# Performance work log

Hardware: AMD Instinct MI355X
Metric: run time of the kernel (lower is better)

The kernel has to match this reference:

```python
import jax, jax.numpy as jnp
import numpy as np
from jax import lax

E = 4      # n_experts
K = 2      # top_k
D = 1024   # d_model
B, S = 4, 4096


def setup_inputs() -> dict:
    key = jax.random.key(0)
    ks = jax.random.split(key, 9)
    sc = 1.0 / np.sqrt(D)
    x = jax.random.normal(ks[0], (B, S, D), dtype=jnp.float32)
    Wg = jax.random.normal(ks[1], (E, D, D), dtype=jnp.float32) * sc
    bg = jax.random.normal(ks[2], (E, D), dtype=jnp.float32) * sc
    Wv = jax.random.normal(ks[3], (E, D, D), dtype=jnp.float32) * sc
    bv = jax.random.normal(ks[4], (E, D), dtype=jnp.float32) * sc
    Wd = jax.random.normal(ks[5], (E, D, D), dtype=jnp.float32) * sc
    # decay_bias_init = 1.0 (torch init.constant_)
    bd = jnp.ones((E, D), dtype=jnp.float32)
    Wgate = jax.random.normal(ks[7], (E, D), dtype=jnp.float32) * sc
    return {"x": x, "Wg": Wg, "bg": bg, "Wv": Wv, "bv": bv,
            "Wd": Wd, "bd": bd, "Wgate": Wgate}


def reference(x, Wg, bg, Wv, bv, Wd, bd, Wgate):
    # Per-expert projections (torch Linear: y = x @ W.T + b; W is (out,in))
    g = jnp.einsum('bsd,eod->ebso', x, Wg) + bg[:, None, None, :]  # (E,B,S,D)
    v = jnp.einsum('bsd,eod->ebso', x, Wv) + bv[:, None, None, :]
    d = jnp.einsum('bsd,eod->ebso', x, Wd) + bd[:, None, None, :]
    x_scan = jax.nn.sigmoid(g) * jnp.tanh(v)
    a = 0.001 + 0.998 * jax.nn.sigmoid(d)

    # Causal linear RNN: h_t = a_t * h_{t-1} + x_t, vectorized over (E,B,D)
    xs = jnp.moveaxis(x_scan, 2, 0)  # (S,E,B,D)
    as_ = jnp.moveaxis(a, 2, 0)      # (S,E,B,D)

    def step(h, inp):
        a_t, x_t = inp
        h = a_t * h + x_t
        return h, h

    h0 = jnp.zeros((E, B, x.shape[-1]), dtype=x.dtype)
    _, outs = lax.scan(step, h0, (as_, xs))        # (S,E,B,D)
    expert_outs = jnp.transpose(outs, (2, 0, 3, 1))  # (B,S,D,E)

    # Router: top-k experts per token, softmax over selected logits
    gate_logits = jnp.einsum('bsd,ed->bse', x, Wgate)  # (B,S,E)
    top_vals, top_idx = lax.top_k(gate_logits, K)      # (B,S,K)
    weights = jax.nn.softmax(top_vals, axis=-1)        # (B,S,K)

    idx = jnp.broadcast_to(top_idx[:, :, None, :],
                           (x.shape[0], x.shape[1], x.shape[2], K))
    selected = jnp.take_along_axis(expert_outs, idx, axis=-1)  # (B,S,D,K)
    return (selected * weights[:, :, None, :]).sum(axis=-1)
```

## Files before the change

### kernel.cpp

```cpp
#include <hip/hip_runtime.h>

#define E_EXP 4
#define D_MODEL 1024
#define B_BATCH 4
#define S_SEQ 4096
#define NTOK (B_BATCH*S_SEQ)
#define CHUNK 32
#define NCHUNK (S_SEQ/CHUNK)

typedef float f4 __attribute__((ext_vector_type(4)));
typedef float f32x4 __attribute__((ext_vector_type(4)));
typedef short bf16x8 __attribute__((ext_vector_type(8)));

__device__ __forceinline__ unsigned short f2b(float f){
  union{float f;unsigned u;}v; v.f=f;
  unsigned r = v.u + 0x7fffu + ((v.u>>16)&1u);
  return (unsigned short)(r>>16);
}
__device__ __forceinline__ float b2f_lo(unsigned v){ union{unsigned u;float f;}x; x.u=v<<16; return x.f; }
__device__ __forceinline__ float b2f_hi(unsigned v){ union{unsigned u;float f;}x; x.u=v&0xffff0000u; return x.f; }

__device__ __forceinline__ void gload_lds16(const void* g, void* l){
  __builtin_amdgcn_global_load_lds(
      (const __attribute__((address_space(1))) void*)g,
      (__attribute__((address_space(3))) void*)l, 16, 0, 0);
}

__global__ __launch_bounds__(256) void cvt_bf16(const float* __restrict__ src,
                                                unsigned short* __restrict__ dst)
{
  size_t i = ((size_t)blockIdx.x*256 + threadIdx.x)*4;
  f4 v = *(const f4*)(src + i);
  ushort4 o; o.x=f2b(v[0]); o.y=f2b(v[1]); o.z=f2b(v[2]); o.w=f2b(v[3]);
  *(ushort4*)(dst + i) = o;
}

__global__ __launch_bounds__(256) void cvt_w3(const float* __restrict__ Wg,
                                              const float* __restrict__ Wv,
                                              const float* __restrict__ Wd,
                                              unsigned short* __restrict__ Wcat,
                                              int e0)
{
  const size_t DD = (size_t)D_MODEL*D_MODEL;
  size_t i4 = ((size_t)blockIdx.x*256 + threadIdx.x)*4;
  size_t le3m = i4 >> 20;
  size_t rem  = i4 & (DD-1);
  int mat = (int)(le3m % 3);
  int le  = (int)(le3m / 3);
  const float* src = (mat==0 ? Wg : (mat==1 ? Wv : Wd)) + (size_t)(e0+le)*DD + rem;
  f4 v = *(const f4*)src;
  ushort4 o; o.x=f2b(v[0]); o.y=f2b(v[1]); o.z=f2b(v[2]); o.w=f2b(v[3]);
  *(ushort4*)(Wcat + le3m*DD + rem) = o;
}

__global__ __launch_bounds__(256) void router_kernel(
    const float* __restrict__ x, const float* __restrict__ Wgate,
    float* __restrict__ wtok)
{
  int gtid = blockIdx.x*256 + threadIdx.x;
  int tok  = gtid >> 6;
  int lane = threadIdx.x & 63;
  const float* xr = x + (size_t)tok * D_MODEL;
  float acc0=0.f,acc1=0.f,acc2=0.f,acc3=0.f;
  for (int k=lane;k<D_MODEL;k+=64){
    float xv = xr[k];
    acc0 += xv*Wgate[0*D_MODEL+k];
    acc1 += xv*Wgate[1*D_MODEL+k];
    acc2 += xv*Wgate[2*D_MODEL+k];
    acc3 += xv*Wgate[3*D_MODEL+k];
  }
  #pragma unroll
  for (int off=32;off>0;off>>=1){
    acc0 += __shfl_down(acc0,off);
    acc1 += __shfl_down(acc1,off);
    acc2 += __shfl_down(acc2,off);
    acc3 += __shfl_down(acc3,off);
  }
  if (lane==0){
    float l[4]={acc0,acc1,acc2,acc3};
    int i1=0;
    #pragma unroll
    for(int e=1;e<4;e++) if (l[e]>l[i1]) i1=e;
    int i2=-1;
    #pragma unroll
    for(int e=0;e<4;e++){ if(e==i1) continue; if(i2<0||l[e]>l[i2]) i2=e; }
    float ex = __expf(l[i2]-l[i1]);
    float w1 = 1.f/(1.f+ex);
    float w2 = ex/(1.f+ex);
    float w[4]={0.f,0.f,0.f,0.f};
    w[i1]=w1; w[i2]=w2;
    float* wp = wtok + (size_t)tok*E_EXP;
    wp[0]=w[0]; wp[1]=w[1]; wp[2]=w[2]; wp[3]=w[3];
  }
}

#define BM 128
#define BN 128
#define BK 32

__global__ __launch_bounds__(256) void gemm_3n(
    const unsigned short* __restrict__ A,
    const unsigned short* __restrict__ Wcat,
    unsigned short* __restrict__ gvd)
{
  __shared__ unsigned short sA[BM*BK];
  __shared__ unsigned short sB[BN*BK];
  const size_t DD = (size_t)D_MODEL*D_MODEL;
  const size_t ND = (size_t)NTOK*D_MODEL;

  int le    = blockIdx.z;
  int mbase = blockIdx.x*BM;
  int ntile = blockIdx.y;
  int mat   = ntile>>3;
  int nbase = (ntile&7)*BN;
  int tid  = threadIdx.x;
  int wave = tid>>6, lane = tid&63;
  int wm = wave>>1, wn = wave&1;

  const unsigned short* Wmat = Wcat + ((size_t)le*3 + mat)*DD;

  int src_chunk = (lane&3) ^ ((lane>>3)&3);
  int srow = lane>>2;
  const unsigned short* gA0 = A    + (size_t)(mbase + wave*32 + srow)*D_MODEL + src_chunk*8;
  const unsigned short* gA1 = gA0  + (size_t)16*D_MODEL;
  const unsigned short* gB0 = Wmat + (size_t)(nbase + wave*32 + srow)*D_MODEL + src_chunk*8;
  const unsigned short* gB1 = gB0  + (size_t)16*D_MODEL;
  unsigned short* lA0 = &sA[(wave*32)*BK];
  unsigned short* lA1 = &sA[(wave*32+16)*BK];
  unsigned short* lB0 = &sB[(wave*32)*BK];
  unsigned short* lB1 = &sB[(wave*32+16)*BK];

  f32x4 acc[4][4];
  #pragma unroll
  for (int i=0;i<4;i++)
    #pragma unroll
    for (int j=0;j<4;j++) acc[i][j] = 0;

  int swiz   = (lane>>1)&3;
  int rd_chk = ((lane>>4) ^ swiz)*8;
  int a_base = (wm*64 + (lane&15))*BK + rd_chk;
  int b_base = (wn*64 + (lane&15))*BK + rd_chk;

  for (int k0=0; k0<D_MODEL; k0+=BK){
    gload_lds16(gA0 + k0, lA0);
    gload_lds16(gA1 + k0, lA1);
    gload_lds16(gB0 + k0, lB0);
    gload_lds16(gB1 + k0, lB1);
    __syncthreads();
    bf16x8 af[4], bfv[4];
    #pragma unroll
    for (int mi=0;mi<4;mi++) af[mi]  = *(const bf16x8*)&sA[a_base + mi*16*BK];
    #pragma unroll
    for (int ni=0;ni<4;ni++) bfv[ni] = *(const bf16x8*)&sB[b_base + ni*16*BK];
    #pragma unroll
    for (int mi=0;mi<4;mi++)
      #pragma unroll
      for (int ni=0;ni<4;ni++)
        acc[mi][ni] = __builtin_amdgcn_mfma_f32_16x16x32_bf16(af[mi], bfv[ni], acc[mi][ni], 0, 0, 0);
    __syncthreads();
  }

  unsigned short* outp = gvd + ((size_t)le*3 + mat)*ND;
  int me = mbase + wm*64;
  int ne = nbase + wn*64;
  #pragma unroll
  for (int mi=0;mi<4;mi++){
    #pragma unroll
    for (int r=0;r<4;r++){
      int m = me + mi*16 + (lane>>4)*4 + r;
      size_t rowoff = (size_t)m*D_MODEL;
      #pragma unroll
      for (int ni=0;ni<4;ni++){
        int n = ne + ni*16 + (lane&15);
        outp[rowoff+n] = f2b(acc[mi][ni][r]);
      }
    }
  }
}

__global__ __launch_bounds__(512) void scan_pass1(
    unsigned short* __restrict__ gvd,
    const float* __restrict__ bg, const float* __restrict__ bv, const float* __restrict__ bd,
    float* __restrict__ P, float* __restrict__ U, int e0)
{
  const size_t ND = (size_t)NTOK*D_MODEL;
  int blk = blockIdx.x;
  int c  = blk % NCHUNK;
  int b  = (blk / NCHUNK) % B_BATCH;
  int le = blk / (NCHUNK*B_BATCH);
  int d0 = threadIdx.x*2;
  int e  = e0 + le;

  float bg0 = bg[(size_t)e*D_MODEL+d0], bg1 = bg[(size_t)e*D_MODEL+d0+1];
  float bv0 = bv[(size_t)e*D_MODEL+d0], bv1 = bv[(size_t)e*D_MODEL+d0+1];
  float bd0 = bd[(size_t)e*D_MODEL+d0], bd1 = bd[(size_t)e*D_MODEL+d0+1];

  unsigned short* gp = gvd + (size_t)le*3*ND;
  size_t base = (((size_t)b)*S_SEQ + (size_t)c*CHUNK)*D_MODEL + d0;
  float h0=0.f,h1=0.f,p0=1.f,p1=1.f;
  for (int t=0;t<CHUNK;t++){
    unsigned gw = *(const unsigned*)(gp + base);
    unsigned vw = *(const unsigned*)(gp + ND + base);
    unsigned dw = *(const unsigned*)(gp + 2*ND + base);
    float g0 = b2f_lo(gw)+bg0, g1 = b2f_hi(gw)+bg1;
    float v0 = b2f_lo(vw)+bv0, v1 = b2f_hi(vw)+bv1;
    float dd0 = b2f_lo(dw)+bd0, dd1 = b2f_hi(dw)+bd1;
    float x0 = (1.f/(1.f+__expf(-g0))) * (1.f - 2.f/(__expf(2.f*v0)+1.f));
    float x1 = (1.f/(1.f+__expf(-g1))) * (1.f - 2.f/(__expf(2.f*v1)+1.f));
    float a0 = 0.001f + 0.998f/(1.f+__expf(-dd0));
    float a1 = 0.001f + 0.998f/(1.f+__expf(-dd1));
    h0 = a0*h0 + x0; h1 = a1*h1 + x1;
    p0 *= a0; p1 *= a1;
    unsigned xsw = (unsigned)f2b(x0) | ((unsigned)f2b(x1)<<16);
    unsigned aaw = (unsigned)f2b(a0) | ((unsigned)f2b(a1)<<16);
    *(unsigned*)(gp + base)        = xsw;
    *(unsigned*)(gp + 2*ND + base) = aaw;
    base += D_MODEL;
  }
  size_t sidx = (((size_t)(le*B_BATCH + b))*NCHUNK + c)*D_MODEL + d0;
  P[sidx]=p0; P[sidx+1]=p1;
  U[sidx]=h0; U[sidx+1]=h1;
}

__global__ __launch_bounds__(256) void scan_pass2(
    const float* __restrict__ P, const float* __restrict__ U, float* __restrict__ Hinit)
{
  int ch = blockIdx.x*256 + threadIdx.x;
  int d  = ch & (D_MODEL-1);
  int eb = ch >> 10;
  size_t base = (size_t)eb*NCHUNK*D_MODEL + d;
  float H=0.f;
  for (int c=0;c<NCHUNK;c++){
    size_t idx = base + (size_t)c*D_MODEL;
    Hinit[idx] = H;
    H = P[idx]*H + U[idx];
  }
}

template<int G, int FIRST>
__global__ __launch_bounds__(512) void scan_pass3(
    const unsigned short* __restrict__ gvd,
    const float* __restrict__ Hinit, const float* __restrict__ wtok,
    float* __restrict__ out, int e0)
{
  const size_t ND = (size_t)NTOK*D_MODEL;
  int blk = blockIdx.x;
  int c = blk % NCHUNK;
  int b = blk / NCHUNK;
  int d0 = threadIdx.x*2;
  float h[G][2];
  #pragma unroll
  for (int le=0; le<G; le++){
    size_t hi = (((size_t)(le*B_BATCH+b))*NCHUNK + c)*D_MODEL + d0;
    h[le][0]=Hinit[hi]; h[le][1]=Hinit[hi+1];
  }
  int s0 = c*CHUNK;
  for (int t=0;t<CHUNK;t++){
    size_t n = (size_t)b*S_SEQ + s0 + t;
    float o0=0.f, o1=0.f;
    #pragma unroll
    for (int le=0;le<G;le++){
      float w = wtok[n*E_EXP + e0 + le];
      size_t idx = (size_t)le*3*ND + n*D_MODEL + d0;
      unsigned xv = *(const unsigned*)(gvd + idx);
      unsigned av = *(const unsigned*)(gvd + 2*ND + idx);
      h[le][0] = b2f_lo(av)*h[le][0] + b2f_lo(xv);
      h[le][1] = b2f_hi(av)*h[le][1] + b2f_hi(xv);
      o0 += w*h[le][0];
      o1 += w*h[le][1];
    }
    float* op = out + n*D_MODEL + d0;
    if (FIRST){ op[0]=o0;  op[1]=o1;  }
    else      { op[0]+=o0; op[1]+=o1; }
  }
}

extern "C" void kernel_launch(void* const* d_in, const int* in_sizes, int n_in,
                              void* d_out, int out_size, void* d_ws, size_t ws_size,
                              hipStream_t stream)
{
  const float* x     = (const float*)d_in[0];
  const float* Wg    = (const float*)d_in[1];
  const float* bg    = (const float*)d_in[2];
  const float* Wv    = (const float*)d_in[3];
  const float* bv    = (const float*)d_in[4];
  const float* Wd    = (const float*)d_in[5];
  const float* bd    = (const float*)d_in[6];
  const float* Wgate = (const float*)d_in[7];
  float* out = (float*)d_out;

  const size_t DD        = (size_t)D_MODEL*D_MODEL;
  const size_t ND        = (size_t)NTOK*D_MODEL;
  const size_t wtok_b    = (size_t)NTOK*E_EXP*4;
  const size_t xbf_b     = ND*2;
  const size_t w_per_e   = 3*DD*2;
  const size_t gvd_per_e = 3*ND*2;
  const size_t st_per_e  = (size_t)B_BATCH*NCHUNK*D_MODEL*4;

  int G = 1;
  for (int g = 4; g >= 1; g >>= 1){
    size_t need = wtok_b + xbf_b + (size_t)g*(w_per_e + gvd_per_e + 3*st_per_e);
    if (need <= ws_size){ G = g; break; }
  }

  char* wsb = (char*)d_ws;
  size_t off = 0;
  float*          wtok = (float*)(wsb+off);          off += wtok_b;
  unsigned short* xbf  = (unsigned short*)(wsb+off); off += xbf_b;
  unsigned short* Wcat = (unsigned short*)(wsb+off); off += (size_t)G*w_per_e;
  unsigned short* gvd  = (unsigned short*)(wsb+off); off += (size_t)G*gvd_per_e;
  float*          P    = (float*)(wsb+off);          off += (size_t)G*st_per_e;
  float*          U    = (float*)(wsb+off);          off += (size_t)G*st_per_e;
  float*          Hi   = (float*)(wsb+off);

  cvt_bf16<<<(unsigned)(ND/1024), 256, 0, stream>>>(x, xbf);
  router_kernel<<<NTOK/4, 256, 0, stream>>>(x, Wgate, wtok);

  for (int e0=0; e0<E_EXP; e0+=G){
    cvt_w3<<<(unsigned)((size_t)G*3*DD/1024), 256, 0, stream>>>(Wg, Wv, Wd, Wcat, e0);

    dim3 gg(NTOK/BM, 3*D_MODEL/BN, G);
    gemm_3n<<<gg, 256, 0, stream>>>(xbf, Wcat, gvd);

    scan_pass1<<<G*B_BATCH*NCHUNK, 512, 0, stream>>>(gvd, bg, bv, bd, P, U, e0);
    scan_pass2<<<G*B_BATCH*D_MODEL/256, 256, 0, stream>>>(P, U, Hi);
    bool first = (e0 == 0);
    if (G==4)      scan_pass3<4,1><<<B_BATCH*NCHUNK, 512, 0, stream>>>(gvd, Hi, wtok, out, e0);
    else if (G==2){
      if (first) scan_pass3<2,1><<<B_BATCH*NCHUNK, 512, 0, stream>>>(gvd, Hi, wtok, out, e0);
      else       scan_pass3<2,0><<<B_BATCH*NCHUNK, 512, 0, stream>>>(gvd, Hi, wtok, out, e0);
    } else {
      if (first) scan_pass3<1,1><<<B_BATCH*NCHUNK, 512, 0, stream>>>(gvd, Hi, wtok, out, e0);
      else       scan_pass3<1,0><<<B_BATCH*NCHUNK, 512, 0, stream>>>(gvd, Hi, wtok, out, e0);
    }
  }
}
```

Baseline: 865.3 us.

## Replace 128x128 GEMM with double-buffered 256x256 tile, 8-wave pipelined kernel

The per-expert projection GEMM moves from a 128x128x32 single-buffered tile with 4 waves to a 256x256x64 tile with 8 waves and two LDS buffers. The K loop is split into quarter-tile windows that interleave async global-to-LDS staging of the next tiles with LDS reads and MFMA work, using explicit waitcnt, barriers and s_setprio. The goals are higher arithmetic intensity per LDS byte and overlap of memory latency with compute. In exchange it uses more registers and 64KB of LDS per block, and relies on delicate hand-written wait counts for correctness.

```diff
diff --git a/kernel.cpp b/kernel.cpp
--- a/kernel.cpp
+++ b/kernel.cpp
@@ -94,84 +94,130 @@
   }
 }
 
-#define BM 128
-#define BN 128
-#define BK 32
-
-__global__ __launch_bounds__(256) void gemm_3n(
+#define BM2 256
+#define BN2 256
+#define BK2 64
+#define NT2 (D_MODEL/BK2)
+
+__global__ __launch_bounds__(512, 2) void gemm256(
     const unsigned short* __restrict__ A,
     const unsigned short* __restrict__ Wcat,
     unsigned short* __restrict__ gvd)
 {
-  __shared__ unsigned short sA[BM*BK];
-  __shared__ unsigned short sB[BN*BK];
+  __shared__ unsigned short sA[2][BM2][BK2];
+  __shared__ unsigned short sB[2][BN2][BK2];
   const size_t DD = (size_t)D_MODEL*D_MODEL;
   const size_t ND = (size_t)NTOK*D_MODEL;
 
-  int le    = blockIdx.z;
-  int mbase = blockIdx.x*BM;
-  int ntile = blockIdx.y;
-  int mat   = ntile>>3;
-  int nbase = (ntile&7)*BN;
-  int tid  = threadIdx.x;
-  int wave = tid>>6, lane = tid&63;
-  int wm = wave>>1, wn = wave&1;
+  const int le    = blockIdx.z;
+  const int mbase = blockIdx.x*BM2;
+  const int ntile = blockIdx.y;
+  const int mat   = ntile>>2;
+  const int nbase = (ntile&3)*BN2;
+
+  const int tid  = threadIdx.x;
+  const int wave = tid>>6, lane = tid&63;
+  const int wm = wave>>2, wn = wave&3;
+  const int l15 = lane&15;
+  const int l8  = lane>>3;
+  const int lc  = (lane&7) ^ l8;
 
   const unsigned short* Wmat = Wcat + ((size_t)le*3 + mat)*DD;
-
-  int src_chunk = (lane&3) ^ ((lane>>3)&3);
-  int srow = lane>>2;
-  const unsigned short* gA0 = A    + (size_t)(mbase + wave*32 + srow)*D_MODEL + src_chunk*8;
-  const unsigned short* gA1 = gA0  + (size_t)16*D_MODEL;
-  const unsigned short* gB0 = Wmat + (size_t)(nbase + wave*32 + srow)*D_MODEL + src_chunk*8;
-  const unsigned short* gB1 = gB0  + (size_t)16*D_MODEL;
-  unsigned short* lA0 = &sA[(wave*32)*BK];
-  unsigned short* lA1 = &sA[(wave*32+16)*BK];
-  unsigned short* lB0 = &sB[(wave*32)*BK];
-  unsigned short* lB1 = &sB[(wave*32+16)*BK];
-
-  f32x4 acc[4][4];
+  const unsigned short* gA = A + (size_t)(mbase + wave*8 + l8)*D_MODEL + lc*8;
+  const int bBw = (wave>>1)*64 + (wave&1)*8;
+  const unsigned short* gB = Wmat + (size_t)(nbase + bBw + l8)*D_MODEL + lc*8;
+
+  const int arow = wm*128 + l15;
+  const int brow = wn*64  + l15;
+  const int ach0 = (((lane>>4)    ) ^ (lane&7))*8;
+  const int ach1 = (((lane>>4) + 4) ^ (lane&7))*8;
+
+  f32x4 acc[8][4];
   #pragma unroll
-  for (int i=0;i<4;i++)
+  for (int i=0;i<8;i++)
     #pragma unroll
     for (int j=0;j<4;j++) acc[i][j] = 0;
 
-  int swiz   = (lane>>1)&3;
-  int rd_chk = ((lane>>4) ^ swiz)*8;
-  int a_base = (wm*64 + (lane&15))*BK + rd_chk;
-  int b_base = (wn*64 + (lane&15))*BK + rd_chk;
-
-  for (int k0=0; k0<D_MODEL; k0+=BK){
-    gload_lds16(gA0 + k0, lA0);
-    gload_lds16(gA1 + k0, lA1);
-    gload_lds16(gB0 + k0, lB0);
-    gload_lds16(gB1 + k0, lB1);
-    __syncthreads();
-    bf16x8 af[4], bfv[4];
-    #pragma unroll
-    for (int mi=0;mi<4;mi++) af[mi]  = *(const bf16x8*)&sA[a_base + mi*16*BK];
-    #pragma unroll
-    for (int ni=0;ni<4;ni++) bfv[ni] = *(const bf16x8*)&sB[b_base + ni*16*BK];
-    #pragma unroll
-    for (int mi=0;mi<4;mi++)
-      #pragma unroll
-      for (int ni=0;ni<4;ni++)
-        acc[mi][ni] = __builtin_amdgcn_mfma_f32_16x16x32_bf16(af[mi], bfv[ni], acc[mi][ni], 0, 0, 0);
-    __syncthreads();
-  }
+  bf16x8 af[4][2], bfv[2][2];
+
+#define STAGE_A2(slot,t,mh) do{ \
+  gload_lds16(gA + (size_t)((mh)*64)*D_MODEL     + (t)*BK2, &sA[slot][(mh)*64 + wave*8][0]); \
+  gload_lds16(gA + (size_t)(128+(mh)*64)*D_MODEL + (t)*BK2, &sA[slot][128+(mh)*64 + wave*8][0]); \
+}while(0)
+#define STAGE_B2(slot,t,nh) do{ \
+  gload_lds16(gB + (size_t)((nh)*32)*D_MODEL    + (t)*BK2, &sB[slot][bBw + (nh)*32][0]); \
+  gload_lds16(gB + (size_t)((nh)*32+16)*D_MODEL + (t)*BK2, &sB[slot][bBw + (nh)*32 + 16][0]); \
+}while(0)
+#define LOAD_A2(slot,mh) do{ \
+  _Pragma("unroll") for (int _m=0;_m<4;++_m){ \
+    af[_m][0] = *(const bf16x8*)&sA[slot][arow + ((mh)*4+_m)*16][ach0]; \
+    af[_m][1] = *(const bf16x8*)&sA[slot][arow + ((mh)*4+_m)*16][ach1]; \
+  } \
+}while(0)
+#define LOAD_B2(slot,nh) do{ \
+  _Pragma("unroll") for (int _n=0;_n<2;++_n){ \
+    bfv[_n][0] = *(const bf16x8*)&sB[slot][brow + ((nh)*2+_n)*16][ach0]; \
+    bfv[_n][1] = *(const bf16x8*)&sB[slot][brow + ((nh)*2+_n)*16][ach1]; \
+  } \
+}while(0)
+#define MQ2(mh,nh) do{ \
+  _Pragma("unroll") for (int _m=0;_m<4;++_m) \
+  _Pragma("unroll") for (int _n=0;_n<2;++_n) \
+  _Pragma("unroll") for (int _k=0;_k<2;++_k) \
+    acc[(mh)*4+_m][(nh)*2+_n] = __builtin_amdgcn_mfma_f32_16x16x32_bf16( \
+        af[_m][_k], bfv[_n][_k], acc[(mh)*4+_m][(nh)*2+_n], 0,0,0); \
+}while(0)
+#define KC_LGKM0  asm volatile("s_waitcnt lgkmcnt(0)" ::: "memory")
+#define KC_LGKM8  asm volatile("s_waitcnt lgkmcnt(8)" ::: "memory")
+#define KC_VM4    asm volatile("s_waitcnt vmcnt(4)" ::: "memory")
+#define BAR       __builtin_amdgcn_s_barrier()
+#define PRIO1     __builtin_amdgcn_s_setprio(1)
+#define PRIO0     __builtin_amdgcn_s_setprio(0)
+
+#define WINDOW2(slot,oslot,T1,T2) do{ \
+  LOAD_A2(slot,0); LOAD_B2(slot,0); \
+  STAGE_A2(oslot,T1,1); STAGE_B2(oslot,T1,0); \
+  KC_LGKM8; BAR; KC_LGKM0; \
+  PRIO1; MQ2(0,0); PRIO0; BAR; \
+  LOAD_B2(slot,1); \
+  BAR; KC_LGKM0; \
+  PRIO1; MQ2(0,1); PRIO0; BAR; \
+  LOAD_A2(slot,1); \
+  STAGE_A2(slot,T2,0); \
+  BAR; KC_LGKM0; \
+  PRIO1; MQ2(1,1); PRIO0; BAR; \
+  LOAD_B2(slot,0); \
+  STAGE_B2(slot,T2,1); \
+  KC_VM4; BAR; KC_LGKM0; \
+  PRIO1; MQ2(1,0); PRIO0; BAR; \
+}while(0)
+
+  STAGE_A2(0,0,0); STAGE_A2(0,0,1); STAGE_B2(0,0,0); STAGE_B2(0,0,1);
+  STAGE_A2(1,1,0); STAGE_B2(1,1,1);
+  KC_VM4; BAR;
+
+  for (int tp=0; tp<NT2/2; ++tp){
+    int ta = 2*tp+1;
+    int tb = 2*tp+2; if (tb>=NT2) tb -= NT2;
+    int tc = 2*tp+3; if (tc>=NT2) tc -= NT2;
+    WINDOW2(0,1,ta,tb);
+    WINDOW2(1,0,tb,tc);
+  }
+
+  asm volatile("s_waitcnt vmcnt(0)" ::: "memory");
 
   unsigned short* outp = gvd + ((size_t)le*3 + mat)*ND;
-  int me = mbase + wm*64;
-  int ne = nbase + wn*64;
+  const int me = mbase + wm*128;
+  const int ne = nbase + wn*64;
   #pragma unroll
-  for (int mi=0;mi<4;mi++){
+  for (int mi=0;mi<8;mi++){
     #pragma unroll
     for (int r=0;r<4;r++){
       int m = me + mi*16 + (lane>>4)*4 + r;
       size_t rowoff = (size_t)m*D_MODEL;
       #pragma unroll
       for (int ni=0;ni<4;ni++){
-        int n = ne + ni*16 + (lane&15);
+        int n = ne + ni*16 + l15;
         outp[rowoff+n] = f2b(acc[mi][ni][r]);
       }
     }
@@ -319,8 +365,8 @@
   for (int e0=0; e0<E_EXP; e0+=G){
     cvt_w3<<<(unsigned)((size_t)G*3*DD/1024), 256, 0, stream>>>(Wg, Wv, Wd, Wcat, e0);
 
-    dim3 gg(NTOK/BM, 3*D_MODEL/BN, G);
-    gemm_3n<<<gg, 256, 0, stream>>>(xbf, Wcat, gvd);
+    dim3 gg(NTOK/BM2, 3*D_MODEL/BN2, G);
+    gemm256<<<gg, 512, 0, stream>>>(xbf, Wcat, gvd);
 
     scan_pass1<<<G*B_BATCH*NCHUNK, 512, 0, stream>>>(gvd, bg, bv, bd, P, U, e0);
     scan_pass2<<<G*B_BATCH*D_MODEL/256, 256, 0, stream>>>(P, U, Hi);
```

Measured after the change: 833.7 us. 3.6% less time.
